# Optimization experiments

Hardware: AMD Instinct MI355X
Metric: run time of the kernel (lower is better)

## Reference

```python
import jax, jax.numpy as jnp
import numpy as np

B, S, D = 4, 2048, 1024

def _xavier(key, shape):
    bound = float(np.sqrt(6.0 / (shape[0] + shape[1])))
    return jax.random.uniform(key, shape, dtype=jnp.float32, minval=-bound, maxval=bound)

def setup_inputs() -> dict:
    key = jax.random.key(0)
    k0, k1, k2, k3 = jax.random.split(key, 4)
    return {
        "embeddings": jax.random.normal(k0, (B, S, D), dtype=jnp.float32),
        "W_Q": _xavier(k1, (D, D)),
        "W_K": _xavier(k2, (D, D)),
        "W_V": _xavier(k3, (D, D)),
    }

def reference(embeddings, W_Q, W_K, W_V):
    _, seq_len, d = embeddings.shape
    Q = embeddings @ W_Q                      # [B,S,D]
    K = embeddings @ W_K
    V = embeddings @ W_V
    scale = 1.0 / jnp.sqrt(jnp.float32(d))
    scores = jnp.einsum('bqd,bkd->bqk', Q, K) * scale   # [B,S,S]
    causal = jnp.tril(jnp.ones((seq_len, seq_len), dtype=bool))
    scores = jnp.where(causal[None, :, :], scores, -jnp.inf)
    probs = jax.nn.softmax(scores, axis=-1)
    return jnp.einsum('bqk,bkd->bqd', probs, V)
```

## Files before the change

kernel.cpp:

```cpp
#include <hip/hip_runtime.h>
#include <hip/hip_bf16.h>

#define BSZ 4
#define SEQ 2048
#define DIM 1024

typedef __attribute__((ext_vector_type(8))) short bf16x8;
typedef __attribute__((ext_vector_type(4))) float floatx4;

__device__ __forceinline__ unsigned short f2bf(float x) {
  union { float f; unsigned int u; } v; v.f = x;
  unsigned int r = v.u + 0x7fffu + ((v.u >> 16) & 1u);
  return (unsigned short)(r >> 16);
}

template <typename T> __device__ __forceinline__ void store_c(T* p, float v);
template <> __device__ __forceinline__ void store_c<float>(float* p, float v) { *p = v; }
template <> __device__ __forceinline__ void store_c<unsigned short>(unsigned short* p, float v) { *p = f2bf(v); }

__global__ __launch_bounds__(256) void prep(const float* __restrict__ E,
                                            const float* __restrict__ Wq,
                                            const float* __restrict__ Wk,
                                            const float* __restrict__ Wv,
                                            unsigned short* __restrict__ Ebf,
                                            unsigned short* __restrict__ WtQK,
                                            unsigned short* __restrict__ WtV,
                                            float* __restrict__ rsum, int n) {
  __shared__ float tile[32][33];
  int b = blockIdx.x;
  int tid = threadIdx.x;
  if (b < 8192) {
    if (b < 8) {
      int j = b * 1024 + tid * 4;
      *(float4*)(rsum + j) = make_float4(0.f, 0.f, 0.f, 0.f);
    }
    int i = (b * 256 + tid) * 4;
    if (i >= n) return;
    float4 v = *(const float4*)(E + i);
    ushort4 o;
    o.x = f2bf(v.x); o.y = f2bf(v.y); o.z = f2bf(v.z); o.w = f2bf(v.w);
    *(ushort4*)(Ebf + i) = o;
  } else {
    b -= 8192;
    int z = b >> 10;
    int rb = b & 1023;
    int bx = rb & 31, by = rb >> 5;
    const float* W = (z == 0) ? Wq : (z == 1) ? Wk : Wv;
    unsigned short* dst = (z == 2) ? WtV : WtQK;
    int row_off = (z == 1) ? 1024 : 0;
    int n0 = bx * 32, k0 = by * 32;
    int tx = tid & 31, ty = tid >> 5;
    for (int r = ty; r < 32; r += 8)
      tile[r][tx] = W[(size_t)(k0 + r) * DIM + n0 + tx];
    __syncthreads();
    for (int r = ty; r < 32; r += 8)
      dst[(size_t)(row_off + n0 + r) * DIM + k0 + tx] = f2bf(tile[tx][r]);
  }
}

__device__ __forceinline__ void gload16(const unsigned short* g, unsigned short* l) {
  __builtin_amdgcn_global_load_lds(
      (const __attribute__((address_space(1))) unsigned int*)g,
      (__attribute__((address_space(3))) unsigned int*)l, 16, 0, 0);
}

template <int MODE = 0>
__device__ __forceinline__ void proj8ph(
    const unsigned short* __restrict__ A, int lda,
    const unsigned short* __restrict__ Bm, int ldb,
    unsigned short* __restrict__ C, int ldc, int m0, int n0,
    unsigned short* sA, unsigned short* sB,
    float scale = 0.f, float* __restrict__ rowsum = nullptr) {
  const int tid = threadIdx.x;
  const int lane = tid & 63;
  const int wid = tid >> 6;
  const int wm = (wid >> 2) * 128;
  const int wn = (wid & 3) * 64;
  const int lr = lane & 15, lq = lane >> 4;

  unsigned short* aB = sA + (wm >> 7) * 8192 + lr * 64;
  unsigned short* bB = sB + (wn >> 7) * 8192 + ((wn & 64) + lr) * 64;
  const int sw0 = (lq ^ (lr & 7)) * 8;
  const int sw1 = ((4 + lq) ^ (lr & 7)) * 8;

  const int schunk = (tid & 7) ^ ((tid >> 3) & 7);
  const unsigned short* gA = A + (size_t)(m0 + (tid >> 3)) * lda + schunk * 8;
  const unsigned short* gB = Bm + (size_t)(n0 + (tid >> 3)) * ldb + schunk * 8;
  unsigned short* lA = sA + wid * 512;
  unsigned short* lB = sB + wid * 512;

#define STG_A(buf, T, half) do { \
    gload16(gA + (size_t)((half) * 128) * lda + (T) * 64,      lA + (buf) * 16384 + (half) * 8192); \
    gload16(gA + (size_t)((half) * 128 + 64) * lda + (T) * 64, lA + (buf) * 16384 + (half) * 8192 + 4096); } while (0)
#define STG_B(buf, T, half) do { \
    gload16(gB + (size_t)((half) * 128) * ldb + (T) * 64,      lB + (buf) * 16384 + (half) * 8192); \
    gload16(gB + (size_t)((half) * 128 + 64) * ldb + (T) * 64, lB + (buf) * 16384 + (half) * 8192 + 4096); } while (0)
#define RD_A(buf, qr) do { _Pragma("unroll") for (int i_ = 0; i_ < 4; ++i_) { \
    af[i_][0] = *(const bf16x8*)(aB + (buf) * 16384 + ((qr) * 64 + i_ * 16) * 64 + sw0); \
    af[i_][1] = *(const bf16x8*)(aB + (buf) * 16384 + ((qr) * 64 + i_ * 16) * 64 + sw1); } } while (0)
#define RD_B(buf, qc) do { _Pragma("unroll") for (int j_ = 0; j_ < 2; ++j_) { \
    bq[qc][j_][0] = *(const bf16x8*)(bB + (buf) * 16384 + ((qc) * 32 + j_ * 16) * 64 + sw0); \
    bq[qc][j_][1] = *(const bf16x8*)(bB + (buf) * 16384 + ((qc) * 32 + j_ * 16) * 64 + sw1); } } while (0)
#define MM(qr, qc) do { __builtin_amdgcn_s_setprio(1); \
    _Pragma("unroll") for (int i_ = 0; i_ < 4; ++i_) \
    _Pragma("unroll") for (int jj_ = 0; jj_ < 2; ++jj_) { \
      acc[(qr)*4+i_][(qc)*2+jj_] = __builtin_amdgcn_mfma_f32_16x16x32_bf16(af[i_][0], bq[qc][jj_][0], acc[(qr)*4+i_][(qc)*2+jj_], 0, 0, 0); \
      acc[(qr)*4+i_][(qc)*2+jj_] = __builtin_amdgcn_mfma_f32_16x16x32_bf16(af[i_][1], bq[qc][jj_][1], acc[(qr)*4+i_][(qc)*2+jj_], 0, 0, 0); } \
    __builtin_amdgcn_s_setprio(0); } while (0)
#define BAR __builtin_amdgcn_s_barrier()
#define LGKM0 do { asm volatile("s_waitcnt lgkmcnt(0)" ::: "memory"); __builtin_amdgcn_sched_barrier(0); } while (0)
#define VM4 asm volatile("s_waitcnt vmcnt(4)" ::: "memory")
#define VM0 asm volatile("s_waitcnt vmcnt(0)" ::: "memory")

  floatx4 acc[8][4] = {};
  bf16x8 af[4][2], bq[2][2][2];

  STG_B(0, 0, 0); STG_B(0, 0, 1);
  STG_A(0, 0, 0); STG_A(0, 0, 1);
  STG_B(1, 1, 0); STG_B(1, 1, 1);
  VM4;
  BAR;

#pragma unroll 1
  for (int j = 0; j < 8; ++j) {
    const int t0 = 2 * j, t1 = 2 * j + 1;
    const bool st = (j < 7);
    RD_A(0, 0); RD_B(0, 0);
    STG_A(1, t1, 0);
    BAR; LGKM0; MM(0, 0); BAR;

    RD_B(0, 1);
    STG_A(1, t1, 1);
    BAR; LGKM0; MM(0, 1); BAR;

    RD_A(0, 1);
    if (st) STG_B(0, t0 + 2, 0);
    BAR; LGKM0; MM(1, 0); BAR;

    if (st) STG_B(0, t0 + 2, 1);
    BAR; MM(1, 1);
    if (st) { VM4; } else { VM0; }
    BAR;

    RD_A(1, 0); RD_B(1, 0);
    if (st) STG_A(0, t0 + 2, 0);
    BAR; LGKM0; MM(0, 0); BAR;

    RD_B(1, 1);
    if (st) STG_A(0, t0 + 2, 1);
    BAR; LGKM0; MM(0, 1); BAR;

    RD_A(1, 1);
    if (st) STG_B(1, t1 + 2, 0);
    BAR; LGKM0; MM(1, 0); BAR;

    if (st) STG_B(1, t1 + 2, 1);
    BAR; MM(1, 1);
    if (st) { VM4; }
    BAR;
  }
#undef STG_A
#undef STG_B
#undef RD_A
#undef RD_B
#undef MM
#undef BAR
#undef LGKM0
#undef VM4
#undef VM0

  if constexpr (MODE == 1) {
#pragma unroll
    for (int i = 0; i < 8; ++i) {
      int rbase = m0 + wm + i * 16 + lq * 4;
      float s0 = 0.f, s1 = 0.f, s2 = 0.f, s3 = 0.f;
#pragma unroll
      for (int jc = 0; jc < 4; ++jc) {
        int col = n0 + wn + jc * 16 + lr;
        float e0 = (col <= rbase + 0) ? __expf(acc[i][jc][0] * scale) : 0.0f;
        float e1 = (col <= rbase + 1) ? __expf(acc[i][jc][1] * scale) : 0.0f;
        float e2 = (col <= rbase + 2) ? __expf(acc[i][jc][2] * scale) : 0.0f;
        float e3 = (col <= rbase + 3) ? __expf(acc[i][jc][3] * scale) : 0.0f;
        C[(size_t)(rbase + 0) * ldc + col] = f2bf(e0);
        C[(size_t)(rbase + 1) * ldc + col] = f2bf(e1);
        C[(size_t)(rbase + 2) * ldc + col] = f2bf(e2);
        C[(size_t)(rbase + 3) * ldc + col] = f2bf(e3);
        s0 += e0; s1 += e1; s2 += e2; s3 += e3;
      }
#pragma unroll
      for (int m = 1; m < 16; m <<= 1) {
        s0 += __shfl_xor(s0, m, 64);
        s1 += __shfl_xor(s1, m, 64);
        s2 += __shfl_xor(s2, m, 64);
        s3 += __shfl_xor(s3, m, 64);
      }
      if (lr == 0) {
        atomicAdd(&rowsum[rbase + 0], s0);
        atomicAdd(&rowsum[rbase + 1], s1);
        atomicAdd(&rowsum[rbase + 2], s2);
        atomicAdd(&rowsum[rbase + 3], s3);
      }
    }
  } else {
#pragma unroll
    for (int i = 0; i < 8; ++i) {
      int rbase = m0 + wm + i * 16 + lq * 4;
#pragma unroll
      for (int jc = 0; jc < 4; ++jc) {
        int col = n0 + wn + jc * 16 + lr;
#pragma unroll
        for (int r = 0; r < 4; ++r)
          C[(size_t)(rbase + r) * ldc + col] = f2bf(acc[i][jc][r]);
      }
    }
  }
}

#define NT_PROJ 32

template <int BMt, int MODE = 0>
__device__ __forceinline__ void proj_core(
    const unsigned short* __restrict__ A, int lda,
    const unsigned short* __restrict__ Bm, int ldb,
    unsigned short* __restrict__ C, int ldc, int m0, int n0,
    unsigned short* sAr, unsigned short* sBr,
    float scale = 0.f, float* __restrict__ rowsum = nullptr) {
  constexpr int LPA = BMt / 128;
  constexpr int LPT = LPA + 2;
  constexpr int FR  = BMt / 32;
  constexpr int TA  = BMt * 32;
  constexpr int TB  = 256 * 32;

  const int tid = threadIdx.x;
  const int lane = tid & 63;
  const int wid = tid >> 6;
  const int wm = (wid >> 2) * (BMt / 2);
  const int wn = (wid & 3) * 64;
  const int lr = lane & 15, lq = lane >> 4;

  const int srow = tid >> 2;
  const int schunk = (tid & 3) ^ ((tid >> 3) & 3);
  const unsigned short* gA = A + (size_t)(m0 + srow) * lda + schunk * 8;
  const unsigned short* gB = Bm + (size_t)(n0 + srow) * ldb + schunk * 8;
  unsigned short* lA = sAr + 16 * 32 * wid;
  unsigned short* lB = sBr + 16 * 32 * wid;
  const size_t swGA = (size_t)128 * lda;
  const size_t swGB = (size_t)128 * ldb;

#define STAGE_A(T) do { int rb_ = (T) & 3; \
    gload16(gA + (size_t)(T) * 32, lA + rb_ * TA); \
    if constexpr (LPA == 2) gload16(gA + (size_t)(T) * 32 + swGA, lA + rb_ * TA + 4096); } while (0)
#define STAGE_B(T) do { int rb_ = (T) & 3; \
    gload16(gB + (size_t)(T) * 32,        lB + rb_ * TB); \
    gload16(gB + (size_t)(T) * 32 + swGB, lB + rb_ * TB + 4096); } while (0)
#define ARD(rb_, rowv) (*(const bf16x8*)&sAr[(rb_) * TA + (rowv) * 32 + (lq ^ (((rowv) >> 1) & 3)) * 8])
#define BRD(rb_, rowv) (*(const bf16x8*)&sBr[(rb_) * TB + (rowv) * 32 + (lq ^ (((rowv) >> 1) & 3)) * 8])

  floatx4 acc[FR][4] = {};

  STAGE_A(0); STAGE_B(0);
  STAGE_A(1); STAGE_B(1);
  STAGE_A(2); STAGE_B(2);
  if constexpr (LPT == 4) asm volatile("s_waitcnt vmcnt(8)" ::: "memory");
  else                    asm volatile("s_waitcnt vmcnt(6)" ::: "memory");
  __builtin_amdgcn_s_barrier();

#pragma unroll 4
  for (int T = 0; T < NT_PROJ; ++T) {
    const int rb = T & 3;
    bf16x8 af[4], bfr[4];
#pragma unroll
    for (int j = 0; j < 4; ++j) bfr[j] = BRD(rb, wn + j * 16 + lr);
#pragma unroll
    for (int i = 0; i < 4; ++i) af[i] = ARD(rb, wm + i * 16 + lr);
    if (T + 3 < NT_PROJ) {
      STAGE_A(T + 3);
      if constexpr (BMt == 128) STAGE_B(T + 3);
    }
    __builtin_amdgcn_s_barrier();
    __builtin_amdgcn_s_setprio(1);
#pragma unroll
    for (int i = 0; i < 4; ++i)
#pragma unroll
      for (int j = 0; j < 4; ++j)
        acc[i][j] = __builtin_amdgcn_mfma_f32_16x16x32_bf16(af[i], bfr[j], acc[i][j], 0, 0, 0);
    __builtin_amdgcn_s_setprio(0);
    if constexpr (BMt == 256) {
      __builtin_amdgcn_s_barrier();
#pragma unroll
      for (int i = 0; i < 4; ++i) af[i] = ARD(rb, wm + 64 + i * 16 + lr);
      if (T + 3 < NT_PROJ) STAGE_B(T + 3);
      __builtin_amdgcn_s_barrier();
      __builtin_amdgcn_s_setprio(1);
#pragma unroll
      for (int i = 0; i < 4; ++i)
#pragma unroll
        for (int j = 0; j < 4; ++j)
          acc[4 + i][j] = __builtin_amdgcn_mfma_f32_16x16x32_bf16(af[i], bfr[j], acc[4 + i][j], 0, 0, 0);
      __builtin_amdgcn_s_setprio(0);
    }
    if (T < NT_PROJ - 3) {
      if constexpr (LPT == 4) asm volatile("s_waitcnt vmcnt(8)" ::: "memory");
      else                    asm volatile("s_waitcnt vmcnt(6)" ::: "memory");
    } else if (T == NT_PROJ - 3) {
      if constexpr (LPT == 4) asm volatile("s_waitcnt vmcnt(4)" ::: "memory");
      else                    asm volatile("s_waitcnt vmcnt(3)" ::: "memory");
    } else if (T == NT_PROJ - 2) {
      asm volatile("s_waitcnt vmcnt(0)" ::: "memory");
    }
    __builtin_amdgcn_s_barrier();
  }
#undef STAGE_A
#undef STAGE_B
#undef ARD
#undef BRD

#pragma unroll
  for (int i = 0; i < FR; ++i) {
    int rbase = m0 + wm + i * 16 + lq * 4;
#pragma unroll
    for (int j = 0; j < 4; ++j) {
      int col = n0 + wn + j * 16 + lr;
#pragma unroll
      for (int r = 0; r < 4; ++r)
        C[(size_t)(rbase + r) * ldc + col] = f2bf(acc[i][j][r]);
    }
  }
}

__global__ __launch_bounds__(512, 2) void proj256(
    const unsigned short* __restrict__ Ebf,
    const unsigned short* __restrict__ WtQK,
    const unsigned short* __restrict__ WtV,
    unsigned short* __restrict__ QKo,
    unsigned short* __restrict__ Vt) {
  __shared__ __align__(16) unsigned short sA[32768];
  __shared__ __align__(16) unsigned short sB[32768];
  int x = blockIdx.x;
  if (x < 256) {
    proj8ph<0>(Ebf, DIM, WtQK, DIM, QKo, 2 * DIM, (x >> 3) * 256, (x & 7) * 256, sA, sB);
  } else {
    x -= 256;
    proj_core<128>(WtV, DIM, Ebf, DIM, Vt, BSZ * SEQ, (x >> 5) * 128, (x & 31) * 256, sA, sB);
  }
}

__global__ __launch_bounds__(512, 2) void scores256(
    const unsigned short* __restrict__ QK,
    unsigned short* __restrict__ ExpS,
    float* __restrict__ Rsum) {
  __shared__ __align__(16) unsigned short sA[32768];
  __shared__ __align__(16) unsigned short sB[32768];
  int t = blockIdx.x;
  int mt = 0;
  while (((mt + 1) * (mt + 2)) / 2 <= t) mt++;
  int nt = t - (mt * (mt + 1)) / 2;
  const unsigned short* A = QK + (size_t)blockIdx.z * SEQ * 2 * DIM;
  proj8ph<1>(A, 2 * DIM, A + DIM, 2 * DIM,
             ExpS + (size_t)blockIdx.z * SEQ * SEQ, SEQ,
             mt * 256, nt * 256, sA, sB,
             0.03125f ,
             Rsum + (size_t)blockIdx.z * SEQ);
}

template <typename OutT, int MODE>
__global__ __launch_bounds__(256, 2) void gemm_ring(
    const unsigned short* __restrict__ A, int lda, long long strideA,
    const unsigned short* __restrict__ B, int ldb, long long strideB,
    OutT* __restrict__ C, int ldc, long long strideC,
    int Kdim, float scale, float* __restrict__ rowsum) {
  int m0, n0;
  if constexpr (MODE == 1) {
    int t = blockIdx.x;
    int mt = 0;
    while (((mt + 1) * (mt + 2)) / 2 <= t) mt++;
    int nt = t - (mt * (mt + 1)) / 2;
    m0 = mt * 128; n0 = nt * 128;
  } else {
    int yy = ((blockIdx.z >> 1) & 1) ? blockIdx.y : (gridDim.y - 1 - blockIdx.y);
    m0 = yy * 128;
    n0 = blockIdx.x * 128;
  }
  const int Keff = (MODE == 2) ? min(Kdim, m0 + 128) : Kdim;
  const int NT = Keff >> 5;
  A += (long long)blockIdx.z * strideA;
  B += (long long)blockIdx.z * strideB;
  C += (long long)blockIdx.z * strideC;
  rowsum += (size_t)blockIdx.z * SEQ;

  __shared__ __align__(16) unsigned short sA[4 * 4096];
  __shared__ __align__(16) unsigned short sB[4 * 4096];

  const int tid = threadIdx.x;
  const int lane = tid & 63;
  const int wid = tid >> 6;
  const int wm = (wid >> 1) * 64, wn = (wid & 1) * 64;
  const int lr = lane & 15, lq = lane >> 4;

  const int schunk = (tid & 3) ^ ((tid >> 3) & 3);
  const unsigned short* gA = A + (size_t)(m0 + (tid >> 2)) * lda + schunk * 8;
  const unsigned short* gB = B + (size_t)(n0 + (tid >> 2)) * ldb + schunk * 8;
  unsigned short* lA = sA + wid * 512;
  unsigned short* lB = sB + wid * 512;
  const size_t sGA = (size_t)64 * lda, sGB = (size_t)64 * ldb;

#define RSTAGE(T) do { int rb_ = (T) & 3; \
    gload16(gA + (size_t)(T) * 32,       lA + rb_ * 4096); \
    gload16(gA + (size_t)(T) * 32 + sGA, lA + rb_ * 4096 + 2048); \
    gload16(gB + (size_t)(T) * 32,       lB + rb_ * 4096); \
    gload16(gB + (size_t)(T) * 32 + sGB, lB + rb_ * 4096 + 2048); } while (0)
#define RARD(rb_, rowv) (*(const bf16x8*)&sA[(rb_) * 4096 + (rowv) * 32 + (lq ^ (((rowv) >> 1) & 3)) * 8])
#define RBRD(rb_, rowv) (*(const bf16x8*)&sB[(rb_) * 4096 + (rowv) * 32 + (lq ^ (((rowv) >> 1) & 3)) * 8])

  floatx4 acc[4][4] = {};

  RSTAGE(0); RSTAGE(1); RSTAGE(2);
  asm volatile("s_waitcnt vmcnt(8)" ::: "memory");
  __builtin_amdgcn_s_barrier();

  for (int T = 0; T < NT; ++T) {
    const int rb = T & 3;
    bf16x8 af[4], bfr[4];
#pragma unroll
    for (int j = 0; j < 4; ++j) bfr[j] = RBRD(rb, wn + j * 16 + lr);
#pragma unroll
    for (int i = 0; i < 4; ++i) af[i] = RARD(rb, wm + i * 16 + lr);
    if (T + 3 < NT) RSTAGE(T + 3);
    __builtin_amdgcn_s_barrier();
    __builtin_amdgcn_s_setprio(1);
#pragma unroll
    for (int i = 0; i < 4; ++i)
#pragma unroll
      for (int j = 0; j < 4; ++j)
        acc[i][j] = __builtin_amdgcn_mfma_f32_16x16x32_bf16(af[i], bfr[j], acc[i][j], 0, 0, 0);
    __builtin_amdgcn_s_setprio(0);
    if (T < NT - 3)       asm volatile("s_waitcnt vmcnt(8)" ::: "memory");
    else if (T == NT - 3) asm volatile("s_waitcnt vmcnt(4)" ::: "memory");
    else if (T == NT - 2) asm volatile("s_waitcnt vmcnt(0)" ::: "memory");
    __builtin_amdgcn_s_barrier();
  }
#undef RSTAGE
#undef RARD
#undef RBRD

  if constexpr (MODE == 1) {
#pragma unroll
    for (int i = 0; i < 4; i++) {
      int rbase = m0 + wm + i * 16 + lq * 4;
      float s0 = 0.f, s1 = 0.f, s2 = 0.f, s3 = 0.f;
#pragma unroll
      for (int j = 0; j < 4; j++) {
        int col = n0 + wn + j * 16 + lr;
        float e0 = (col <= rbase + 0) ? __expf(acc[i][j][0] * scale) : 0.0f;
        float e1 = (col <= rbase + 1) ? __expf(acc[i][j][1] * scale) : 0.0f;
        float e2 = (col <= rbase + 2) ? __expf(acc[i][j][2] * scale) : 0.0f;
        float e3 = (col <= rbase + 3) ? __expf(acc[i][j][3] * scale) : 0.0f;
        store_c(&C[(size_t)(rbase + 0) * ldc + col], e0);
        store_c(&C[(size_t)(rbase + 1) * ldc + col], e1);
        store_c(&C[(size_t)(rbase + 2) * ldc + col], e2);
        store_c(&C[(size_t)(rbase + 3) * ldc + col], e3);
        s0 += e0; s1 += e1; s2 += e2; s3 += e3;
      }
#pragma unroll
      for (int m = 1; m < 16; m <<= 1) {
        s0 += __shfl_xor(s0, m, 64);
        s1 += __shfl_xor(s1, m, 64);
        s2 += __shfl_xor(s2, m, 64);
        s3 += __shfl_xor(s3, m, 64);
      }
      if (lr == 0) {
        atomicAdd(&rowsum[rbase + 0], s0);
        atomicAdd(&rowsum[rbase + 1], s1);
        atomicAdd(&rowsum[rbase + 2], s2);
        atomicAdd(&rowsum[rbase + 3], s3);
      }
    }
  } else {
#pragma unroll
    for (int i = 0; i < 4; i++) {
      int rbase = m0 + wm + i * 16 + lq * 4;
      float i0 = 1.0f / rowsum[rbase + 0];
      float i1 = 1.0f / rowsum[rbase + 1];
      float i2 = 1.0f / rowsum[rbase + 2];
      float i3 = 1.0f / rowsum[rbase + 3];
#pragma unroll
      for (int j = 0; j < 4; j++) {
        int col = n0 + wn + j * 16 + lr;
        store_c(&C[(size_t)(rbase + 0) * ldc + col], acc[i][j][0] * i0);
        store_c(&C[(size_t)(rbase + 1) * ldc + col], acc[i][j][1] * i1);
        store_c(&C[(size_t)(rbase + 2) * ldc + col], acc[i][j][2] * i2);
        store_c(&C[(size_t)(rbase + 3) * ldc + col], acc[i][j][3] * i3);
      }
    }
  }
}

extern "C" void kernel_launch(void* const* d_in, const int* in_sizes, int n_in,
                              void* d_out, int out_size, void* d_ws, size_t ws_size,
                              hipStream_t stream) {
  const float* E  = (const float*)d_in[0];
  const float* Wq = (const float*)d_in[1];
  const float* Wk = (const float*)d_in[2];
  const float* Wv = (const float*)d_in[3];
  float* out = (float*)d_out;

  char* ws = (char*)d_ws;
  size_t off = 0;
  auto alloc = [&](size_t bytes) {
    void* p = ws + off;
    off += (bytes + 255) & ~(size_t)255;
    return p;
  };
  const size_t M_ALL = (size_t)BSZ * SEQ;
  unsigned short* Ebf  = (unsigned short*)alloc(M_ALL * DIM * 2);
  unsigned short* WtQK = (unsigned short*)alloc((size_t)2 * DIM * DIM * 2);
  unsigned short* WtV  = (unsigned short*)alloc((size_t)DIM * DIM * 2);
  unsigned short* QK   = (unsigned short*)alloc(M_ALL * 2 * DIM * 2);
  unsigned short* Vt   = (unsigned short*)alloc((size_t)DIM * M_ALL * 2);
  unsigned short* ExpS = (unsigned short*)alloc((size_t)BSZ * SEQ * SEQ * 2);
  float*          Rsum = (float*)alloc((size_t)BSZ * SEQ * 4);

  int nE = (int)(M_ALL * DIM);
  prep<<<dim3(11264), dim3(256), 0, stream>>>(E, Wq, Wk, Wv, Ebf, WtQK, WtV, Rsum, nE);

  proj256<<<dim3(512), dim3(512), 0, stream>>>(Ebf, WtQK, WtV, QK, Vt);

  scores256<<<dim3(36, 1, BSZ), dim3(512), 0, stream>>>(QK, ExpS, Rsum);

  gemm_ring<float, 2><<<dim3(8, 16, BSZ), dim3(256), 0, stream>>>(
      ExpS, SEQ, (long long)SEQ * SEQ,
      Vt, (int)M_ALL, (long long)SEQ,
      out, DIM, (long long)SEQ * DIM,
      SEQ, 1.0f, Rsum);
}
```

Before: 225.3 us.

## Fold W_Q·W_Kᵀ into one matrix to replace Q and K projections

```diff
diff --git a/kernel.cpp b/kernel.cpp
--- a/kernel.cpp
+++ b/kernel.cpp
@@ -12,6 +12,17 @@
   union { float f; unsigned int u; } v; v.f = x;
   unsigned int r = v.u + 0x7fffu + ((v.u >> 16) & 1u);
   return (unsigned short)(r >> 16);
+}
+
+__device__ __forceinline__ uint4 ld8f(const float* p) {
+  float4 a = *(const float4*)p;
+  float4 b = *(const float4*)(p + 4);
+  uint4 u;
+  u.x = (unsigned)f2bf(a.x) | ((unsigned)f2bf(a.y) << 16);
+  u.y = (unsigned)f2bf(a.z) | ((unsigned)f2bf(a.w) << 16);
+  u.z = (unsigned)f2bf(b.x) | ((unsigned)f2bf(b.y) << 16);
+  u.w = (unsigned)f2bf(b.z) | ((unsigned)f2bf(b.w) << 16);
+  return u;
 }
 
 template <typename T> __device__ __forceinline__ void store_c(T* p, float v);
@@ -23,38 +34,109 @@
                                             const float* __restrict__ Wk,
                                             const float* __restrict__ Wv,
                                             unsigned short* __restrict__ Ebf,
-                                            unsigned short* __restrict__ WtQK,
                                             unsigned short* __restrict__ WtV,
-                                            float* __restrict__ rsum, int n) {
-  __shared__ float tile[32][33];
+                                            unsigned short* __restrict__ Mt,
+                                            float* __restrict__ rsum) {
+  __shared__ __align__(16) unsigned short As[128][72];
+  __shared__ __align__(16) unsigned short Bs[128][72];
   int b = blockIdx.x;
   int tid = threadIdx.x;
-  if (b < 8192) {
-    if (b < 8) {
-      int j = b * 1024 + tid * 4;
+
+  if (b < 64) {
+    int m0 = (b >> 3) * 128, n0 = (b & 7) * 128;
+    int lane = tid & 63;
+    int wid = tid >> 6;
+    int wm = (wid >> 1) * 64, wn = (wid & 1) * 64;
+    int lr = lane & 15, lq = lane >> 4;
+    int row = tid >> 3;
+    int kc = (tid & 7) * 8;
+
+    const float* Ab = Wk + (size_t)(m0 + row) * DIM + kc;
+    const float* Bb = Wq + (size_t)(n0 + row) * DIM + kc;
+    size_t la = (size_t)32 * DIM;
+
+    uint4 ra0 = ld8f(Ab);
+    uint4 ra1 = ld8f(Ab + la);
+    uint4 ra2 = ld8f(Ab + 2 * la);
+    uint4 ra3 = ld8f(Ab + 3 * la);
+    uint4 rb0 = ld8f(Bb);
+    uint4 rb1 = ld8f(Bb + la);
+    uint4 rb2 = ld8f(Bb + 2 * la);
+    uint4 rb3 = ld8f(Bb + 3 * la);
+
+    floatx4 acc[4][4] = {};
+
+    for (int k0 = 0; k0 < DIM; k0 += 64) {
+      __syncthreads();
+      *(uint4*)&As[row][kc]      = ra0;
+      *(uint4*)&As[row + 32][kc] = ra1;
+      *(uint4*)&As[row + 64][kc] = ra2;
+      *(uint4*)&As[row + 96][kc] = ra3;
+      *(uint4*)&Bs[row][kc]      = rb0;
+      *(uint4*)&Bs[row + 32][kc] = rb1;
+      *(uint4*)&Bs[row + 64][kc] = rb2;
+      *(uint4*)&Bs[row + 96][kc] = rb3;
+      if (k0 + 64 < DIM) {
+        const float* An = Ab + k0 + 64;
+        const float* Bn = Bb + k0 + 64;
+        ra0 = ld8f(An);
+        ra1 = ld8f(An + la);
+        ra2 = ld8f(An + 2 * la);
+        ra3 = ld8f(An + 3 * la);
+        rb0 = ld8f(Bn);
+        rb1 = ld8f(Bn + la);
+        rb2 = ld8f(Bn + 2 * la);
+        rb3 = ld8f(Bn + 3 * la);
+      }
+      __syncthreads();
+#pragma unroll
+      for (int kk = 0; kk < 64; kk += 32) {
+        bf16x8 af[4], bfr[4];
+        int kl = kk + lq * 8;
+#pragma unroll
+        for (int i = 0; i < 4; i++) af[i] = *(const bf16x8*)&As[wm + i * 16 + lr][kl];
+#pragma unroll
+        for (int j = 0; j < 4; j++) bfr[j] = *(const bf16x8*)&Bs[wn + j * 16 + lr][kl];
+#pragma unroll
+        for (int i = 0; i < 4; i++)
+#pragma unroll
+          for (int j = 0; j < 4; j++)
+            acc[i][j] = __builtin_amdgcn_mfma_f32_16x16x32_bf16(af[i], bfr[j], acc[i][j], 0, 0, 0);
+      }
+    }
+#pragma unroll
+    for (int i = 0; i < 4; i++) {
+      int rbase = m0 + wm + i * 16 + lq * 4;
+#pragma unroll
+      for (int j = 0; j < 4; j++) {
+        int col = n0 + wn + j * 16 + lr;
+#pragma unroll
+        for (int r = 0; r < 4; r++)
+          Mt[(size_t)(rbase + r) * DIM + col] = f2bf(acc[i][j][r]);
+      }
+    }
+  } else if (b < 8256) {
+    int base = b - 64;
+    if (base < 8) {
+      int j = base * 1024 + tid * 4;
       *(float4*)(rsum + j) = make_float4(0.f, 0.f, 0.f, 0.f);
     }
-    int i = (b * 256 + tid) * 4;
-    if (i >= n) return;
+    int i = (base * 256 + tid) * 4;
     float4 v = *(const float4*)(E + i);
     ushort4 o;
     o.x = f2bf(v.x); o.y = f2bf(v.y); o.z = f2bf(v.z); o.w = f2bf(v.w);
     *(ushort4*)(Ebf + i) = o;
   } else {
-    b -= 8192;
-    int z = b >> 10;
-    int rb = b & 1023;
+    float* tileF = (float*)As;
+    int rb = b - 8256;
     int bx = rb & 31, by = rb >> 5;
-    const float* W = (z == 0) ? Wq : (z == 1) ? Wk : Wv;
-    unsigned short* dst = (z == 2) ? WtV : WtQK;
-    int row_off = (z == 1) ? 1024 : 0;
     int n0 = bx * 32, k0 = by * 32;
     int tx = tid & 31, ty = tid >> 5;
     for (int r = ty; r < 32; r += 8)
-      tile[r][tx] = W[(size_t)(k0 + r) * DIM + n0 + tx];
+      tileF[r * 33 + tx] = Wv[(size_t)(k0 + r) * DIM + n0 + tx];
     __syncthreads();
     for (int r = ty; r < 32; r += 8)
-      dst[(size_t)(row_off + n0 + r) * DIM + k0 + tx] = f2bf(tile[tx][r]);
+      WtV[(size_t)(n0 + r) * DIM + k0 + tx] = f2bf(tileF[tx * 33 + r]);
   }
 }
 
@@ -216,137 +298,26 @@
   }
 }
 
-#define NT_PROJ 32
-
-template <int BMt, int MODE = 0>
-__device__ __forceinline__ void proj_core(
-    const unsigned short* __restrict__ A, int lda,
-    const unsigned short* __restrict__ Bm, int ldb,
-    unsigned short* __restrict__ C, int ldc, int m0, int n0,
-    unsigned short* sAr, unsigned short* sBr,
-    float scale = 0.f, float* __restrict__ rowsum = nullptr) {
-  constexpr int LPA = BMt / 128;
-  constexpr int LPT = LPA + 2;
-  constexpr int FR  = BMt / 32;
-  constexpr int TA  = BMt * 32;
-  constexpr int TB  = 256 * 32;
-
-  const int tid = threadIdx.x;
-  const int lane = tid & 63;
-  const int wid = tid >> 6;
-  const int wm = (wid >> 2) * (BMt / 2);
-  const int wn = (wid & 3) * 64;
-  const int lr = lane & 15, lq = lane >> 4;
-
-  const int srow = tid >> 2;
-  const int schunk = (tid & 3) ^ ((tid >> 3) & 3);
-  const unsigned short* gA = A + (size_t)(m0 + srow) * lda + schunk * 8;
-  const unsigned short* gB = Bm + (size_t)(n0 + srow) * ldb + schunk * 8;
-  unsigned short* lA = sAr + 16 * 32 * wid;
-  unsigned short* lB = sBr + 16 * 32 * wid;
-  const size_t swGA = (size_t)128 * lda;
-  const size_t swGB = (size_t)128 * ldb;
-
-#define STAGE_A(T) do { int rb_ = (T) & 3; \
-    gload16(gA + (size_t)(T) * 32, lA + rb_ * TA); \
-    if constexpr (LPA == 2) gload16(gA + (size_t)(T) * 32 + swGA, lA + rb_ * TA + 4096); } while (0)
-#define STAGE_B(T) do { int rb_ = (T) & 3; \
-    gload16(gB + (size_t)(T) * 32,        lB + rb_ * TB); \
-    gload16(gB + (size_t)(T) * 32 + swGB, lB + rb_ * TB + 4096); } while (0)
-#define ARD(rb_, rowv) (*(const bf16x8*)&sAr[(rb_) * TA + (rowv) * 32 + (lq ^ (((rowv) >> 1) & 3)) * 8])
-#define BRD(rb_, rowv) (*(const bf16x8*)&sBr[(rb_) * TB + (rowv) * 32 + (lq ^ (((rowv) >> 1) & 3)) * 8])
-
-  floatx4 acc[FR][4] = {};
-
-  STAGE_A(0); STAGE_B(0);
-  STAGE_A(1); STAGE_B(1);
-  STAGE_A(2); STAGE_B(2);
-  if constexpr (LPT == 4) asm volatile("s_waitcnt vmcnt(8)" ::: "memory");
-  else                    asm volatile("s_waitcnt vmcnt(6)" ::: "memory");
-  __builtin_amdgcn_s_barrier();
-
-#pragma unroll 4
-  for (int T = 0; T < NT_PROJ; ++T) {
-    const int rb = T & 3;
-    bf16x8 af[4], bfr[4];
-#pragma unroll
-    for (int j = 0; j < 4; ++j) bfr[j] = BRD(rb, wn + j * 16 + lr);
-#pragma unroll
-    for (int i = 0; i < 4; ++i) af[i] = ARD(rb, wm + i * 16 + lr);
-    if (T + 3 < NT_PROJ) {
-      STAGE_A(T + 3);
-      if constexpr (BMt == 128) STAGE_B(T + 3);
-    }
-    __builtin_amdgcn_s_barrier();
-    __builtin_amdgcn_s_setprio(1);
-#pragma unroll
-    for (int i = 0; i < 4; ++i)
-#pragma unroll
-      for (int j = 0; j < 4; ++j)
-        acc[i][j] = __builtin_amdgcn_mfma_f32_16x16x32_bf16(af[i], bfr[j], acc[i][j], 0, 0, 0);
-    __builtin_amdgcn_s_setprio(0);
-    if constexpr (BMt == 256) {
-      __builtin_amdgcn_s_barrier();
-#pragma unroll
-      for (int i = 0; i < 4; ++i) af[i] = ARD(rb, wm + 64 + i * 16 + lr);
-      if (T + 3 < NT_PROJ) STAGE_B(T + 3);
-      __builtin_amdgcn_s_barrier();
-      __builtin_amdgcn_s_setprio(1);
-#pragma unroll
-      for (int i = 0; i < 4; ++i)
-#pragma unroll
-        for (int j = 0; j < 4; ++j)
-          acc[4 + i][j] = __builtin_amdgcn_mfma_f32_16x16x32_bf16(af[i], bfr[j], acc[4 + i][j], 0, 0, 0);
-      __builtin_amdgcn_s_setprio(0);
-    }
-    if (T < NT_PROJ - 3) {
-      if constexpr (LPT == 4) asm volatile("s_waitcnt vmcnt(8)" ::: "memory");
-      else                    asm volatile("s_waitcnt vmcnt(6)" ::: "memory");
-    } else if (T == NT_PROJ - 3) {
-      if constexpr (LPT == 4) asm volatile("s_waitcnt vmcnt(4)" ::: "memory");
-      else                    asm volatile("s_waitcnt vmcnt(3)" ::: "memory");
-    } else if (T == NT_PROJ - 2) {
-      asm volatile("s_waitcnt vmcnt(0)" ::: "memory");
-    }
-    __builtin_amdgcn_s_barrier();
-  }
-#undef STAGE_A
-#undef STAGE_B
-#undef ARD
-#undef BRD
-
-#pragma unroll
-  for (int i = 0; i < FR; ++i) {
-    int rbase = m0 + wm + i * 16 + lq * 4;
-#pragma unroll
-    for (int j = 0; j < 4; ++j) {
-      int col = n0 + wn + j * 16 + lr;
-#pragma unroll
-      for (int r = 0; r < 4; ++r)
-        C[(size_t)(rbase + r) * ldc + col] = f2bf(acc[i][j][r]);
-    }
-  }
-}
-
-__global__ __launch_bounds__(512, 2) void proj256(
+__global__ __launch_bounds__(512, 2) void bulk8(
     const unsigned short* __restrict__ Ebf,
-    const unsigned short* __restrict__ WtQK,
     const unsigned short* __restrict__ WtV,
-    unsigned short* __restrict__ QKo,
-    unsigned short* __restrict__ Vt) {
+    const unsigned short* __restrict__ Mt,
+    unsigned short* __restrict__ Vt,
+    unsigned short* __restrict__ EM) {
   __shared__ __align__(16) unsigned short sA[32768];
   __shared__ __align__(16) unsigned short sB[32768];
   int x = blockIdx.x;
-  if (x < 256) {
-    proj8ph<0>(Ebf, DIM, WtQK, DIM, QKo, 2 * DIM, (x >> 3) * 256, (x & 7) * 256, sA, sB);
+  if (x < 128) {
+    proj8ph<0>(WtV, DIM, Ebf, DIM, Vt, BSZ * SEQ, (x >> 5) * 256, (x & 31) * 256, sA, sB);
   } else {
-    x -= 256;
-    proj_core<128>(WtV, DIM, Ebf, DIM, Vt, BSZ * SEQ, (x >> 5) * 128, (x & 31) * 256, sA, sB);
+    x -= 128;
+    proj8ph<0>(Ebf, DIM, Mt, DIM, EM, DIM, (x >> 2) * 256, (x & 3) * 256, sA, sB);
   }
 }
 
 __global__ __launch_bounds__(512, 2) void scores256(
-    const unsigned short* __restrict__ QK,
+    const unsigned short* __restrict__ EM,
+    const unsigned short* __restrict__ Ebf,
     unsigned short* __restrict__ ExpS,
     float* __restrict__ Rsum) {
   __shared__ __align__(16) unsigned short sA[32768];
@@ -355,8 +326,9 @@
   int mt = 0;
   while (((mt + 1) * (mt + 2)) / 2 <= t) mt++;
   int nt = t - (mt * (mt + 1)) / 2;
-  const unsigned short* A = QK + (size_t)blockIdx.z * SEQ * 2 * DIM;
-  proj8ph<1>(A, 2 * DIM, A + DIM, 2 * DIM,
+  const unsigned short* A = EM + (size_t)blockIdx.z * SEQ * DIM;
+  const unsigned short* B = Ebf + (size_t)blockIdx.z * SEQ * DIM;
+  proj8ph<1>(A, DIM, B, DIM,
              ExpS + (size_t)blockIdx.z * SEQ * SEQ, SEQ,
              mt * 256, nt * 256, sA, sB,
              0.03125f ,
@@ -513,19 +485,18 @@
   };
   const size_t M_ALL = (size_t)BSZ * SEQ;
   unsigned short* Ebf  = (unsigned short*)alloc(M_ALL * DIM * 2);
-  unsigned short* WtQK = (unsigned short*)alloc((size_t)2 * DIM * DIM * 2);
   unsigned short* WtV  = (unsigned short*)alloc((size_t)DIM * DIM * 2);
-  unsigned short* QK   = (unsigned short*)alloc(M_ALL * 2 * DIM * 2);
+  unsigned short* Mt   = (unsigned short*)alloc((size_t)DIM * DIM * 2);
+  unsigned short* EM   = (unsigned short*)alloc(M_ALL * DIM * 2);
   unsigned short* Vt   = (unsigned short*)alloc((size_t)DIM * M_ALL * 2);
   unsigned short* ExpS = (unsigned short*)alloc((size_t)BSZ * SEQ * SEQ * 2);
   float*          Rsum = (float*)alloc((size_t)BSZ * SEQ * 4);
 
-  int nE = (int)(M_ALL * DIM);
-  prep<<<dim3(11264), dim3(256), 0, stream>>>(E, Wq, Wk, Wv, Ebf, WtQK, WtV, Rsum, nE);
-
-  proj256<<<dim3(512), dim3(512), 0, stream>>>(Ebf, WtQK, WtV, QK, Vt);
-
-  scores256<<<dim3(36, 1, BSZ), dim3(512), 0, stream>>>(QK, ExpS, Rsum);
+  prep<<<dim3(9280), dim3(256), 0, stream>>>(E, Wq, Wk, Wv, Ebf, WtV, Mt, Rsum);
+
+  bulk8<<<dim3(256), dim3(512), 0, stream>>>(Ebf, WtV, Mt, Vt, EM);
+
+  scores256<<<dim3(36, 1, BSZ), dim3(512), 0, stream>>>(EM, Ebf, ExpS, Rsum);
 
   gemm_ring<float, 2><<<dim3(8, 16, BSZ), dim3(256), 0, stream>>>(
       ExpS, SEQ, (long long)SEQ * SEQ,
```

New measurement: 221.5 us. No clear change (-1.7%).
